# Optimization experiments

Measured on AMD Instinct MI355X. Metric: run time of the kernel, lower is better.

Reference implementation:

```python
import jax, jax.numpy as jnp
import numpy as np

N, E, IN, H0, H1 = 50000, 1600000, 64, 64, 128


def _gcn(h, W, b, row, col):
    # PyG GCNConv, add_self_loops=False, unit edge weights:
    # out[col] += d^{-1/2}[row] * d^{-1/2}[col] * (h @ W)[row]; bias added after aggregation
    n = h.shape[0]
    deg = jnp.zeros((n,), h.dtype).at[col].add(jnp.ones((row.shape[0],), h.dtype))
    dinv = jnp.where(deg > 0, jax.lax.rsqrt(jnp.maximum(deg, 1e-12)), 0.0)
    norm = (dinv[row] * dinv[col])[:, None]  # [E,1]
    m = h @ W  # transform before propagate (small GEMM)
    out = jnp.zeros((n, W.shape[1]), h.dtype).at[col].add(norm * m[row])
    return out + b


def _bn(h, g, b):
    # BatchNorm1d training-mode math (biased variance), eps=1e-5
    mu = h.mean(0)
    var = ((h - mu) ** 2).mean(0)
    return g * (h - mu) * jax.lax.rsqrt(var + 1e-5) + b


def _san(h):
    return jnp.nan_to_num(h, nan=0.0, posinf=100.0, neginf=-100.0)


def _slice(x, ei, W0, b0, W1, b1, res1, g0, be0, g1, be1):
    row, col = ei[0], ei[1]
    # layer 0: conv -> bn -> relu -> (dropout=eval identity) -> residual (Identity, 64==64) -> nan_to_num
    h1 = _san(jax.nn.relu(_bn(_gcn(x, W0, b0, row, col), g0, be0)) + x)
    # layer 1 (last): conv -> bn -> residual (Linear proj 64->128, no bias) -> nan_to_num
    h2 = _san(_bn(_gcn(h1, W1, b1, row, col), g1, be1) + h1 @ res1)
    return h2


def setup_inputs() -> dict:
    k = jax.random.split(jax.random.key(0), 16)
    f = lambda kk, sh, s: jax.random.normal(kk, sh, jnp.float32) * s
    return {
        "x": f(k[0], (N, IN), 1.0),
        "edge_index0": jax.random.randint(k[1], (2, E), 0, N),
        "edge_index1": jax.random.randint(k[2], (2, E), 0, N),
        "w0_s0": f(k[3], (IN, H0), 0.1), "b0_s0": jnp.zeros((H0,), jnp.float32),
        "w1_s0": f(k[4], (H0, H1), 0.1), "b1_s0": jnp.zeros((H1,), jnp.float32),
        "res1_s0": f(k[5], (H0, H1), 0.1),
        "w0_s1": f(k[6], (IN, H0), 0.1), "b0_s1": jnp.zeros((H0,), jnp.float32),
        "w1_s1": f(k[7], (H0, H1), 0.1), "b1_s1": jnp.zeros((H1,), jnp.float32),
        "res1_s1": f(k[8], (H0, H1), 0.1),
        "bn_g0": jnp.ones((H0,), jnp.float32), "bn_b0": jnp.zeros((H0,), jnp.float32),
        "bn_g1": jnp.ones((H1,), jnp.float32), "bn_b1": jnp.zeros((H1,), jnp.float32),
        "fc1_w": f(k[9], (2 * H1, H1), 0.1), "fc1_b": jnp.zeros((H1,), jnp.float32),
        "fc2_w": f(k[10], (H1, 2), 0.1), "fc2_b": jnp.zeros((2,), jnp.float32),
    }


def reference(x, edge_index0, edge_index1,
              w0_s0, b0_s0, w1_s0, b1_s0, res1_s0,
              w0_s1, b0_s1, w1_s1, b1_s1, res1_s1,
              bn_g0, bn_b0, bn_g1, bn_b1,
              fc1_w, fc1_b, fc2_w, fc2_b):
    out0 = _slice(x, edge_index0, w0_s0, b0_s0, w1_s0, b1_s0, res1_s0, bn_g0, bn_b0, bn_g1, bn_b1)
    out1 = _slice(x, edge_index1, w0_s1, b0_s1, w1_s1, b1_s1, res1_s1, bn_g0, bn_b0, bn_g1, bn_b1)
    combined = jnp.concatenate([out0, out1], axis=1)  # [N, 2*H1]
    h = jax.nn.relu(combined @ fc1_w + fc1_b)  # dropout is eval-mode identity
    logits = h @ fc2_w + fc2_b
    return logits, jax.nn.softmax(logits, axis=1)
```

## Files before the change

### kernel.cpp

```cpp
#include <hip/hip_runtime.h>
#include <hip/hip_bf16.h>
#include <math.h>


typedef short v8s __attribute__((ext_vector_type(8)));
typedef float f32x4 __attribute__((ext_vector_type(4)));

#define BSTRIDE 10240

__device__ __forceinline__ float sanf(float v) {
    if (v != v) return 0.f;
    if (isinf(v)) return v > 0.f ? 100.f : -100.f;
    return v;
}

__device__ __forceinline__ unsigned short bf16of(float v) {
    __hip_bfloat16 h = __float2bfloat16(v);
    return *(unsigned short*)&h;
}
__device__ __forceinline__ unsigned pack2(float lo, float hi) {
    return (unsigned)bf16of(lo) | ((unsigned)bf16of(hi) << 16);
}
__device__ __forceinline__ float uflo(unsigned u) { return __uint_as_float(u << 16); }
__device__ __forceinline__ float ufhi(unsigned u) { return __uint_as_float(u & 0xFFFF0000u); }
__device__ __forceinline__ float fofbf16(unsigned short u) {
    return __uint_as_float(((unsigned)u) << 16);
}

__device__ __forceinline__ void packone(const float* __restrict__ src, unsigned* __restrict__ dst,
                                        int L, int Khalf, int F) {
    int c = L / Khalf, kp = L - c * Khalf;
    dst[L] = pack2(src[(2 * kp) * F + c], src[(2 * kp + 1) * F + c]);
}

__global__ __launch_bounds__(256) void prep_kernel(const float* __restrict__ w0_0,
                                                   const float* __restrict__ w0_1,
                                                   const float* __restrict__ w1_0,
                                                   const float* __restrict__ w1_1,
                                                   const float* __restrict__ r_0,
                                                   const float* __restrict__ r_1,
                                                   const float* __restrict__ fc1,
                                                   unsigned* __restrict__ wpk,
                                                   int* __restrict__ bcnt,
                                                   float* __restrict__ sums) {
    int gid = blockIdx.x * 256 + threadIdx.x;
    if (gid < 512) bcnt[gid] = 0;
    if (gid < 8192) sums[gid] = 0.f;
    if (gid < 2048)       packone(w0_0, wpk + 0,     gid - 0,     32, 64);
    else if (gid < 4096)  packone(w0_1, wpk + 2048,  gid - 2048,  32, 64);
    else if (gid < 8192)  packone(w1_0, wpk + 4096,  gid - 4096,  32, 128);
    else if (gid < 12288) packone(w1_1, wpk + 8192,  gid - 8192,  32, 128);
    else if (gid < 16384) packone(r_0,  wpk + 12288, gid - 12288, 32, 128);
    else if (gid < 20480) packone(r_1,  wpk + 16384, gid - 16384, 32, 128);
    else if (gid < 36864) packone(fc1,  wpk + 20480, gid - 20480, 128, 128);
}


__global__ __launch_bounds__(512) void kC_bin(const int* __restrict__ ei0,
                                              const int* __restrict__ ei1,
                                              int* __restrict__ bcnt,
                                              unsigned* __restrict__ binned,
                                              int E, int n) {
    __shared__ int cnt[512];
    __shared__ int base[512];
    int t = threadIdx.x;
    cnt[t] = 0;
    int E2 = 2 * E;
    int e0 = blockIdx.x * 8192;
    unsigned pk[16];
    int bk[16];
    __syncthreads();
#pragma unroll
    for (int j = 0; j < 16; ++j) {
        int ge = e0 + t + j * 512;
        bk[j] = -1;
        if (ge < E2) {
            int slice = ge >= E;
            const int* ei = slice ? ei1 : ei0;
            int e = ge - slice * E;
            int col = ei[E + e], row = ei[e];
            int gcol = slice * n + col;
            bk[j] = gcol >> 8;
            pk[j] = (unsigned)row | (((unsigned)gcol & 255u) << 16);
            atomicAdd(&cnt[bk[j]], 1);
        }
    }
    __syncthreads();
    {
        int c = cnt[t];
        base[t] = c ? atomicAdd(&bcnt[t], c) : 0;
    }
    __syncthreads();
    cnt[t] = 0;
    __syncthreads();
#pragma unroll
    for (int j = 0; j < 16; ++j) {
        if (bk[j] >= 0) {
            int loc = atomicAdd(&cnt[bk[j]], 1);
            int off = base[bk[j]] + loc;
            if (off < BSTRIDE) binned[(size_t)bk[j] * BSTRIDE + off] = pk[j];
        }
    }
}

__global__ __launch_bounds__(512) void kD_build(const unsigned* __restrict__ binned,
                                                const int* __restrict__ bcnt,
                                                int* __restrict__ rowptr,
                                                float* __restrict__ dinv,
                                                unsigned short* __restrict__ csr,
                                                int n2, int NB) {
    __shared__ int pref[512];
    __shared__ int cnt[256];
    __shared__ int scn[256];
    __shared__ int cur[256];
    int b = blockIdx.x, t = threadIdx.x;
    pref[t] = (t < NB) ? bcnt[t] : 0;
    __syncthreads();
    for (int off = 1; off < 512; off <<= 1) {
        int u = (t >= off) ? pref[t - off] : 0;
        __syncthreads();
        pref[t] += u;
        __syncthreads();
    }
    int s = (b > 0) ? pref[b - 1] : 0;
    int e = pref[b];
    int m = e - s;
    const unsigned* seg = binned + (size_t)b * BSTRIDE;
    if (t < 256) cnt[t] = 0;
    __syncthreads();
    for (int i = t; i < m; i += 512) atomicAdd(&cnt[(seg[i] >> 16) & 255], 1);
    __syncthreads();
    int v = (t < 256) ? cnt[t] : 0;
    if (t < 256) scn[t] = v;
    __syncthreads();
    for (int off = 1; off < 256; off <<= 1) {
        int u = (t < 256 && t >= off) ? scn[t - off] : 0;
        __syncthreads();
        if (t < 256) scn[t] += u;
        __syncthreads();
    }
    if (t < 256) {
        int excl = scn[t] - v;
        int gcol = b * 256 + t;
        if (gcol < n2) {
            rowptr[gcol] = s + excl;
            dinv[gcol] = v > 0 ? rsqrtf((float)v) : 0.f;
        }
        cur[t] = excl;
    }
    __syncthreads();
    for (int i = t; i < m; i += 512) {
        unsigned p = seg[i];
        int cl = (p >> 16) & 255;
        int pos = s + atomicAdd(&cur[cl], 1);
        csr[pos] = (unsigned short)(p & 0xFFFFu);
    }
    if (b == 0 && t == 0) rowptr[n2] = pref[NB - 1];
}


__global__ __launch_bounds__(256) void prescale_bf(const float* __restrict__ x,
                                                   const float* __restrict__ dinv,
                                                   unsigned short* __restrict__ xsb,
                                                   int n64, int n) {
    int i8 = (blockIdx.x * 256 + threadIdx.x) * 8;
    if (i8 >= n64) return;
    int row = i8 >> 6;
    float4 v0 = *(const float4*)&x[i8];
    float4 v1 = *(const float4*)&x[i8 + 4];
    float d0 = dinv[row], d1 = dinv[n + row];
    uint4 o0, o1;
    o0.x = pack2(v0.x * d0, v0.y * d0); o0.y = pack2(v0.z * d0, v0.w * d0);
    o0.z = pack2(v1.x * d0, v1.y * d0); o0.w = pack2(v1.z * d0, v1.w * d0);
    o1.x = pack2(v0.x * d1, v0.y * d1); o1.y = pack2(v0.z * d1, v0.w * d1);
    o1.z = pack2(v1.x * d1, v1.y * d1); o1.w = pack2(v1.z * d1, v1.w * d1);
    *(uint4*)&xsb[i8] = o0;
    *(uint4*)&xsb[n64 + i8] = o1;
}

#define LOAD8(U, IDX)                                                       \
    do {                                                                    \
        _Pragma("unroll") for (int j = 0; j < 8; ++j) {                     \
            int r = __shfl((IDX), j, 8);                                    \
            (U)[j] = *(const uint4*)&mb[(size_t)r * 64 + l * 8];            \
        }                                                                   \
    } while (0)
#define ZPAD8(U, BB)                                                        \
    do {                                                                    \
        _Pragma("unroll") for (int j = 0; j < 8; ++j)                       \
            if ((BB) + j >= e) { (U)[j].x = 0; (U)[j].y = 0;                \
                                 (U)[j].z = 0; (U)[j].w = 0; }              \
    } while (0)
#define ACC8(U)                                                             \
    do {                                                                    \
        _Pragma("unroll") for (int j = 0; j < 8; ++j) {                     \
            a0 += uflo((U)[j].x); a1 += ufhi((U)[j].x);                     \
            a2 += uflo((U)[j].y); a3 += ufhi((U)[j].y);                     \
            a4 += uflo((U)[j].z); a5 += ufhi((U)[j].z);                     \
            a6 += uflo((U)[j].w); a7 += ufhi((U)[j].w);                     \
        }                                                                   \
    } while (0)

__device__ __forceinline__ void gather_node(const int* __restrict__ rowptr,
                                            const unsigned short* __restrict__ csr,
                                            const unsigned short* __restrict__ mb,
                                            const float* __restrict__ dinv,
                                            int node, int l,
                                            unsigned short* __restrict__ dstrow) {
    int s = rowptr[node], e = rowptr[node + 1];
    float a0 = 0.f, a1 = 0.f, a2 = 0.f, a3 = 0.f, a4 = 0.f, a5 = 0.f, a6 = 0.f, a7 = 0.f;
    uint4 uA[8], uB[8];
    int b = s;
    if (b + 8 <= e) {
        int ia = csr[b + l];
        LOAD8(uA, ia);
        int bB = b + 8;
        int ib = (bB + l < e) ? (int)csr[bB + l] : 0;
        while (true) {
            bool hasB = (bB < e);
            if (hasB) {
                LOAD8(uB, ib);
                if (bB + 8 > e) ZPAD8(uB, bB);
            }
            int bA2 = bB + 8;
            if (bA2 < e) ia = (bA2 + l < e) ? (int)csr[bA2 + l] : 0;
            ACC8(uA);
            if (!hasB) break;
            bool hasA2 = (bA2 < e);
            if (hasA2) {
                LOAD8(uA, ia);
                if (bA2 + 8 > e) ZPAD8(uA, bA2);
            }
            int bB2 = bA2 + 8;
            if (bB2 < e) ib = (bB2 + l < e) ? (int)csr[bB2 + l] : 0;
            ACC8(uB);
            if (!hasA2) break;
            bB = bB2;
        }
    } else if (b < e) {
        int ia = (b + l < e) ? (int)csr[b + l] : 0;
        LOAD8(uA, ia);
        ZPAD8(uA, b);
        ACC8(uA);
    }
    float d = dinv[node];
    uint4 o;
    o.x = pack2(a0 * d, a1 * d);
    o.y = pack2(a2 * d, a3 * d);
    o.z = pack2(a4 * d, a5 * d);
    o.w = pack2(a6 * d, a7 * d);
    *(uint4*)&dstrow[l * 8] = o;
}

template <int F>
__global__ __launch_bounds__(256) void gather_gemmb(const int* __restrict__ rowptr,
                                                    const unsigned short* __restrict__ csr,
                                                    const unsigned short* __restrict__ xsb,
                                                    const float* __restrict__ dinv,
                                                    const unsigned* __restrict__ WT0,
                                                    const unsigned* __restrict__ WT1,
                                                    unsigned short* __restrict__ Cb,
                                                    float* __restrict__ sums_base,
                                                    int roff, int n, int BPS) {
    constexpr int NC = F / 16;
    __shared__ unsigned short at[64 * 72];
    __shared__ unsigned short stb[64 * F];
    __shared__ float ls[2 * F];
    int blk = blockIdx.x;
    int xcd = blk & 7;
    int slice = (xcd >= 4) ? 1 : 0;
    int sb = (blk >> 3) * 4 + (xcd & 3);
    if (sb >= BPS) return;
    const unsigned* WT = slice ? WT1 : WT0;
    int row0 = slice * n + sb * 64;
    int rows = min(64, n - sb * 64);
    int grp = threadIdx.x >> 3, l = threadIdx.x & 7;
    const unsigned short* mb = xsb + (size_t)slice * n * 64;
#pragma unroll
    for (int half = 0; half < 2; ++half) {
        int lr = grp + half * 32;
        if (lr < rows) {
            gather_node(rowptr, csr, mb, dinv, row0 + lr, l, &at[lr * 72]);
        } else {
            uint4 z; z.x = 0; z.y = 0; z.z = 0; z.w = 0;
            *(uint4*)&at[lr * 72 + l * 8] = z;
        }
    }
    for (int i = threadIdx.x; i < 2 * F; i += 256) ls[i] = 0.f;
    __syncthreads();
    int w = threadIdx.x >> 6, lane = threadIdx.x & 63, q = lane >> 4, ln = lane & 15;
    int arow = (16 * w + ln) * 72;
    v8s af0 = *(const v8s*)&at[arow + q * 8];
    v8s af1 = *(const v8s*)&at[arow + 32 + q * 8];
    f32x4 acc[NC];
#pragma unroll
    for (int ct = 0; ct < NC; ++ct) acc[ct] = {0.f, 0.f, 0.f, 0.f};
#pragma unroll
    for (int ct = 0; ct < NC; ++ct) {
        v8s b0 = *(const v8s*)&WT[(ct * 16 + ln) * 32 + q * 4];
        v8s b1 = *(const v8s*)&WT[(ct * 16 + ln) * 32 + 16 + q * 4];
        acc[ct] = __builtin_amdgcn_mfma_f32_16x16x32_bf16(af0, b0, acc[ct], 0, 0, 0);
        acc[ct] = __builtin_amdgcn_mfma_f32_16x16x32_bf16(af1, b1, acc[ct], 0, 0, 0);
    }
#pragma unroll
    for (int ct = 0; ct < NC; ++ct) {
        float s1 = 0.f, s2 = 0.f;
        int cc = ct * 16 + ln;
#pragma unroll
        for (int i = 0; i < 4; ++i) {
            int r = 16 * w + q * 4 + i;
            stb[r * F + (cc ^ ((r & 7) << 3))] = bf16of(acc[ct][i]);
            if (r < rows) {
                float v = acc[ct][i];
                s1 += v;
                s2 += v * v;
            }
        }
        s1 += __shfl_xor(s1, 16); s1 += __shfl_xor(s1, 32);
        s2 += __shfl_xor(s2, 16); s2 += __shfl_xor(s2, 32);
        if (q == 0) {
            atomicAdd(&ls[cc], s1);
            atomicAdd(&ls[F + cc], s2);
        }
    }
    __syncthreads();
    {
        constexpr int CPT = F / 4;
        int rr = threadIdx.x >> 2, sg = threadIdx.x & 3;
        if (rr < rows) {
            int swz = (rr & 7) << 3;
            int cb = sg * CPT;
            uint4* dst = (uint4*)(Cb + (size_t)(row0 + rr) * F + cb);
#pragma unroll
            for (int jj = 0; jj < CPT / 8; ++jj)
                dst[jj] = *(const uint4*)&stb[rr * F + ((cb + jj * 8) ^ swz)];
        }
    }
    if (threadIdx.x < F) {
        float* dst = sums_base + (blockIdx.x & 7) * 1024 + roff + slice * 2 * F;
        unsafeAtomicAdd(&dst[threadIdx.x], ls[threadIdx.x]);
        unsafeAtomicAdd(&dst[F + threadIdx.x], ls[F + threadIdx.x]);
    }
}

__global__ __launch_bounds__(256) void mfma_apply1(const unsigned short* __restrict__ h1b,
                                                   const unsigned short* __restrict__ Tb,
                                                   const unsigned* __restrict__ RT0,
                                                   const unsigned* __restrict__ RT1,
                                                   const float* __restrict__ sums_base,
                                                   const float* __restrict__ g,
                                                   const float* __restrict__ be,
                                                   unsigned short* __restrict__ comb, int n) {
    __shared__ float st[64 * 128];
    __shared__ float scl[256];
    int BPS = (n + 63) >> 6;
    int slice = blockIdx.x >= BPS;
    int sb = blockIdx.x - slice * BPS;
    const unsigned* WT = slice ? RT1 : RT0;
    int row0 = slice * n + sb * 64;
    int rows = min(64, n - sb * 64);
    int t = threadIdx.x;
    if (t < 128) {
        float s1 = 0.f, s2 = 0.f;
#pragma unroll
        for (int r = 0; r < 8; ++r) {
            const float* src = sums_base + r * 1024 + slice * 256;
            s1 += src[t];
            s2 += src[128 + t];
        }
        float inv_n = 1.0f / (float)n;
        float mu = s1 * inv_n;
        float var = fmaxf(s2 * inv_n - mu * mu, 0.f);
        float scale = g[t] * rsqrtf(var + 1e-5f);
        scl[t] = scale;
        scl[128 + t] = be[t] - mu * scale;
    }
    int w = t >> 6, lane = t & 63, q = lane >> 4, ln = lane & 15;
    const unsigned* A32 = (const unsigned*)h1b;
    size_t arow = (size_t)(row0 + 16 * w + ln) * 32;
    v8s af0 = *(const v8s*)&A32[arow + q * 4];
    v8s af1 = *(const v8s*)&A32[arow + 16 + q * 4];
    f32x4 acc[8];
#pragma unroll
    for (int ct = 0; ct < 8; ++ct) acc[ct] = {0.f, 0.f, 0.f, 0.f};
#pragma unroll
    for (int ct = 0; ct < 8; ++ct) {
        v8s b0 = *(const v8s*)&WT[(ct * 16 + ln) * 32 + q * 4];
        v8s b1 = *(const v8s*)&WT[(ct * 16 + ln) * 32 + 16 + q * 4];
        acc[ct] = __builtin_amdgcn_mfma_f32_16x16x32_bf16(af0, b0, acc[ct], 0, 0, 0);
        acc[ct] = __builtin_amdgcn_mfma_f32_16x16x32_bf16(af1, b1, acc[ct], 0, 0, 0);
    }
#pragma unroll
    for (int ct = 0; ct < 8; ++ct) {
        int cc = ct * 16 + ln;
#pragma unroll
        for (int i = 0; i < 4; ++i) {
            int r = 16 * w + q * 4 + i;
            st[r * 128 + (cc ^ ((r & 7) << 2))] = acc[ct][i];
        }
    }
    __syncthreads();
    int rr = t >> 2, sg = t & 3;
    if (rr >= rows) return;
    int swz = (rr & 7) << 2;
    int rg = row0 + rr;
    const uint4* tbp = (const uint4*)(Tb + (size_t)rg * 128 + sg * 32);
    const float* scb = scl + sg * 32;
    uint4* outp = (uint4*)(comb + (size_t)(rg - slice * n) * 256 + slice * 128 + sg * 32);
#pragma unroll
    for (int jj = 0; jj < 4; ++jj) {
        uint4 tv = tbp[jj];
        int base = sg * 32 + jj * 8;
        float4 a0 = *(const float4*)&st[rr * 128 + (base ^ swz)];
        float4 a1 = *(const float4*)&st[rr * 128 + ((base + 4) ^ swz)];
        float4 s0 = *(const float4*)&scb[jj * 8];
        float4 s1 = *(const float4*)&scb[jj * 8 + 4];
        float4 h0 = *(const float4*)&scb[128 + jj * 8];
        float4 h1v = *(const float4*)&scb[128 + jj * 8 + 4];
        float o0 = sanf(fmaf(uflo(tv.x), s0.x, h0.x) + a0.x);
        float o1 = sanf(fmaf(ufhi(tv.x), s0.y, h0.y) + a0.y);
        float o2 = sanf(fmaf(uflo(tv.y), s0.z, h0.z) + a0.z);
        float o3 = sanf(fmaf(ufhi(tv.y), s0.w, h0.w) + a0.w);
        float o4 = sanf(fmaf(uflo(tv.z), s1.x, h1v.x) + a1.x);
        float o5 = sanf(fmaf(ufhi(tv.z), s1.y, h1v.y) + a1.y);
        float o6 = sanf(fmaf(uflo(tv.w), s1.z, h1v.z) + a1.z);
        float o7 = sanf(fmaf(ufhi(tv.w), s1.w, h1v.w) + a1.w);
        uint4 ov;
        ov.x = pack2(o0, o1);
        ov.y = pack2(o2, o3);
        ov.z = pack2(o4, o5);
        ov.w = pack2(o6, o7);
        outp[jj] = ov;
    }
}

__global__ __launch_bounds__(256) void mfma_head_fc2(const unsigned short* __restrict__ comb,
                                                     const unsigned* __restrict__ FT,
                                                     const float* __restrict__ bias,
                                                     const float* __restrict__ w2,
                                                     const float* __restrict__ b2,
                                                     float* __restrict__ out, int n) {
    int row0 = blockIdx.x * 64;
    int rows = min(64, n - row0);
    int w = threadIdx.x >> 6, lane = threadIdx.x & 63, q = lane >> 4, ln = lane & 15;
    const unsigned* A32 = (const unsigned*)comb;
    size_t arow = (size_t)(row0 + 16 * w + ln) * 128;
    f32x4 acc[8];
#pragma unroll
    for (int ct = 0; ct < 8; ++ct) acc[ct] = {0.f, 0.f, 0.f, 0.f};
#pragma unroll
    for (int kt = 0; kt < 4; ++kt) {
        v8s af0 = *(const v8s*)&A32[arow + kt * 32 + q * 4];
        v8s af1 = *(const v8s*)&A32[arow + kt * 32 + 16 + q * 4];
#pragma unroll
        for (int ct = 0; ct < 8; ++ct) {
            v8s b0 = *(const v8s*)&FT[(ct * 16 + ln) * 128 + kt * 32 + q * 4];
            v8s b1 = *(const v8s*)&FT[(ct * 16 + ln) * 128 + kt * 32 + 16 + q * 4];
            acc[ct] = __builtin_amdgcn_mfma_f32_16x16x32_bf16(af0, b0, acc[ct], 0, 0, 0);
            acc[ct] = __builtin_amdgcn_mfma_f32_16x16x32_bf16(af1, b1, acc[ct], 0, 0, 0);
        }
    }
    float p0[4] = {0.f, 0.f, 0.f, 0.f}, p1[4] = {0.f, 0.f, 0.f, 0.f};
#pragma unroll
    for (int ct = 0; ct < 8; ++ct) {
        int c = ct * 16 + ln;
        float bi = bias[c];
        float w20 = w2[c * 2], w21 = w2[c * 2 + 1];
#pragma unroll
        for (int i = 0; i < 4; ++i) {
            float h = fmaxf(acc[ct][i] + bi, 0.f);
            p0[i] = fmaf(h, w20, p0[i]);
            p1[i] = fmaf(h, w21, p1[i]);
        }
    }
#pragma unroll
    for (int i = 0; i < 4; ++i) {
#pragma unroll
        for (int msk = 1; msk < 16; msk <<= 1) {
            p0[i] += __shfl_xor(p0[i], msk);
            p1[i] += __shfl_xor(p1[i], msk);
        }
    }
    if (ln == 0) {
        float bb0 = b2[0], bb1 = b2[1];
#pragma unroll
        for (int i = 0; i < 4; ++i) {
            int r = 16 * w + q * 4 + i;
            if (r >= rows) continue;
            int R = row0 + r;
            float l0 = p0[i] + bb0, l1 = p1[i] + bb1;
            float mx = fmaxf(l0, l1);
            float e0 = expf(l0 - mx), e1 = expf(l1 - mx);
            float inv = 1.0f / (e0 + e1);
            out[(size_t)R * 2] = l0;
            out[(size_t)R * 2 + 1] = l1;
            out[(size_t)2 * n + R * 2] = e0 * inv;
            out[(size_t)2 * n + R * 2 + 1] = e1 * inv;
        }
    }
}

__global__ __launch_bounds__(256) void apply0_kernel(const unsigned short* __restrict__ t0b,
                                                     const float* __restrict__ x,
                                                     const float* __restrict__ sums_base,
                                                     const float* __restrict__ g,
                                                     const float* __restrict__ be,
                                                     const float* __restrict__ dinv,
                                                     unsigned short* __restrict__ h1b,
                                                     unsigned short* __restrict__ h1sb,
                                                     int n64, int total, int n) {
    __shared__ float sc[256];
    int t = threadIdx.x;
    if (t < 128) {
        int slice = t >> 6, f = t & 63;
        float s1 = 0.f, s2 = 0.f;
#pragma unroll
        for (int r = 0; r < 8; ++r) {
            const float* src = sums_base + r * 1024 + 512 + slice * 128;
            s1 += src[f];
            s2 += src[64 + f];
        }
        float inv_n = 1.0f / (float)n;
        float mu = s1 * inv_n;
        float var = fmaxf(s2 * inv_n - mu * mu, 0.f);
        float scale = g[f] * rsqrtf(var + 1e-5f);
        sc[slice * 128 + f] = scale;
        sc[slice * 128 + 64 + f] = be[f] - mu * scale;
    }
    __syncthreads();
    int i8 = (blockIdx.x * 256 + t) * 8;
    if (i8 >= total) return;
    int slice = i8 >= n64;
    int f0 = i8 & 63;
    const float* scp = sc + slice * 128;
    uint4 tv = *(const uint4*)&t0b[i8];
    const float* xp = x + (i8 - slice * n64);
    float4 x0 = *(const float4*)xp;
    float4 x1 = *(const float4*)(xp + 4);
    float4 s0 = *(const float4*)&scp[f0];
    float4 s1 = *(const float4*)&scp[f0 + 4];
    float4 g0 = *(const float4*)&scp[64 + f0];
    float4 g1 = *(const float4*)&scp[64 + f0 + 4];
    float d = dinv[i8 >> 6];
    float tvv[8] = {uflo(tv.x), ufhi(tv.x), uflo(tv.y), ufhi(tv.y),
                    uflo(tv.z), ufhi(tv.z), uflo(tv.w), ufhi(tv.w)};
    float sa[8] = {s0.x, s0.y, s0.z, s0.w, s1.x, s1.y, s1.z, s1.w};
    float sh[8] = {g0.x, g0.y, g0.z, g0.w, g1.x, g1.y, g1.z, g1.w};
    float xv[8] = {x0.x, x0.y, x0.z, x0.w, x1.x, x1.y, x1.z, x1.w};
    unsigned po[4], ps[4];
#pragma unroll
    for (int j = 0; j < 4; ++j) {
        float a = sanf(fmaxf(fmaf(tvv[2 * j], sa[2 * j], sh[2 * j]), 0.f) + xv[2 * j]);
        float b = sanf(fmaxf(fmaf(tvv[2 * j + 1], sa[2 * j + 1], sh[2 * j + 1]), 0.f) + xv[2 * j + 1]);
        po[j] = pack2(a, b);
        ps[j] = pack2(a * d, b * d);
    }
    *(uint4*)&h1b[i8] = *(uint4*)po;
    *(uint4*)&h1sb[i8] = *(uint4*)ps;
}

static inline int cdiv(int a, int b) { return (a + b - 1) / b; }

extern "C" void kernel_launch(void* const* d_in, const int* in_sizes, int n_in,
                              void* d_out, int out_size, void* d_ws, size_t ws_size,
                              hipStream_t stream) {
    const float* x       = (const float*)d_in[0];
    const int*   ei0     = (const int*)d_in[1];
    const int*   ei1     = (const int*)d_in[2];
    const float* w0_s0   = (const float*)d_in[3];
    const float* w1_s0   = (const float*)d_in[5];
    const float* res1_s0 = (const float*)d_in[7];
    const float* w0_s1   = (const float*)d_in[8];
    const float* w1_s1   = (const float*)d_in[10];
    const float* res1_s1 = (const float*)d_in[12];
    const float* bn_g0   = (const float*)d_in[13];
    const float* bn_b0   = (const float*)d_in[14];
    const float* bn_g1   = (const float*)d_in[15];
    const float* bn_b1   = (const float*)d_in[16];
    const float* fc1_w   = (const float*)d_in[17];
    const float* fc1_b   = (const float*)d_in[18];
    const float* fc2_w   = (const float*)d_in[19];
    const float* fc2_b   = (const float*)d_in[20];
    float* out = (float*)d_out;

    int n = in_sizes[0] / 64;
    int E = in_sizes[1] / 2;
    int n2 = 2 * n, E2 = 2 * E;
    int n64 = n * 64;
    int NB = cdiv(n2, 256);
    int BPS = cdiv(n, 64);
    int GG = 8 * cdiv(BPS, 4);

    float* X1 = (float*)d_ws;
    float* S  = X1 + (size_t)n2 * 64;
    unsigned short* Gb   = (unsigned short*)(S + (size_t)n2 * 64);
    unsigned short* h1b  = Gb + (size_t)n2 * 64;
    unsigned short* comb = h1b + (size_t)n2 * 64;
    unsigned short* xsb  = comb + (size_t)n * 256;
    float* dinv = (float*)(xsb + (size_t)n * 128);
    float* sums = dinv + n2;
    float* scsh = sums + 8192;
    unsigned* wpk = (unsigned*)(scsh + 512);
    unsigned short* csr = (unsigned short*)(wpk + 36864);
    int* rowptr = (int*)(csr + (size_t)E2);
    int* bcnt   = rowptr + (n2 + 1);
    unsigned short* t0b = (unsigned short*)X1;
    unsigned short* Tb  = (unsigned short*)X1;
    unsigned* binned = (unsigned*)comb;
    unsigned short* h1sb = (unsigned short*)S;
    unsigned* w0T0 = wpk + 0,    *w0T1 = wpk + 2048;
    unsigned* w1T0 = wpk + 4096, *w1T1 = wpk + 8192;
    unsigned* rT0  = wpk + 12288,*rT1  = wpk + 16384;
    unsigned* fT   = wpk + 20480;

    prep_kernel<<<144, 256, 0, stream>>>(w0_s0, w0_s1, w1_s0, w1_s1,
                                         res1_s0, res1_s1, fc1_w, wpk, bcnt, sums);
    kC_bin<<<cdiv(E2, 8192), 512, 0, stream>>>(ei0, ei1, bcnt, binned, E, n);
    kD_build<<<NB, 512, 0, stream>>>(binned, bcnt, rowptr, dinv, csr, n2, NB);

    prescale_bf<<<cdiv(n64, 2048), 256, 0, stream>>>(x, dinv, xsb, n64, n);
    gather_gemmb<64><<<GG, 256, 0, stream>>>(rowptr, csr, xsb, dinv, w0T0, w0T1,
                                             t0b, sums, 512, n, BPS);
    apply0_kernel<<<cdiv(2 * n64, 2048), 256, 0, stream>>>(t0b, x, sums, bn_g0, bn_b0,
                                                           dinv, h1b, h1sb, n64, 2 * n64, n);

    gather_gemmb<128><<<GG, 256, 0, stream>>>(rowptr, csr, h1sb, dinv, w1T0, w1T1,
                                              Tb, sums, 0, n, BPS);
    mfma_apply1<<<2 * BPS, 256, 0, stream>>>(h1b, Tb, rT0, rT1, sums, bn_g1, bn_b1, comb, n);

    mfma_head_fc2<<<BPS, 256, 0, stream>>>(comb, fT, fc1_b, fc2_w, fc2_b, out, n);
}
```

Baseline: 371.1 us.

## Split fused gather+GEMM into separate gather kernel and MFMA GEMM kernel

Replaces the fused gather_gemmb kernel, which gathered neighbour rows into LDS and then ran MFMA, with two kernels: a standalone gather kernel that writes the aggregated bf16 rows to a global buffer, and an MFMA GEMM that reads A fragments straight from global memory. The gather now runs at 32 nodes per block with no LDS, which may raise occupancy and decouple the latency-bound gather from the GEMM. In exchange it adds an extra global round trip for the aggregated features and two more kernel launches.

```diff
diff --git a/kernel.cpp b/kernel.cpp
--- a/kernel.cpp
+++ b/kernel.cpp
@@ -201,12 +201,21 @@
         }                                                                   \
     } while (0)
 
-__device__ __forceinline__ void gather_node(const int* __restrict__ rowptr,
-                                            const unsigned short* __restrict__ csr,
-                                            const unsigned short* __restrict__ mb,
-                                            const float* __restrict__ dinv,
-                                            int node, int l,
-                                            unsigned short* __restrict__ dstrow) {
+__global__ __launch_bounds__(256) void gatherbf_kernel(const int* __restrict__ rowptr,
+                                                       const unsigned short* __restrict__ csr,
+                                                       const unsigned short* __restrict__ xsb,
+                                                       const float* __restrict__ dinv,
+                                                       unsigned short* __restrict__ outb,
+                                                       int n) {
+    int blk = blockIdx.x;
+    int xcd = blk & 7;
+    int slice = (xcd >= 4) ? 1 : 0;
+    int rank = (blk >> 3) * 4 + (xcd & 3);
+    int nodeLocal = rank * 32 + (threadIdx.x >> 3);
+    if (nodeLocal >= n) return;
+    int node = slice * n + nodeLocal;
+    int l = threadIdx.x & 7;
+    const unsigned short* mb = xsb + (size_t)slice * n * 64;
     int s = rowptr[node], e = rowptr[node + 1];
     float a0 = 0.f, a1 = 0.f, a2 = 0.f, a3 = 0.f, a4 = 0.f, a5 = 0.f, a6 = 0.f, a7 = 0.f;
     uint4 uA[8], uB[8];
@@ -249,49 +258,32 @@
     o.y = pack2(a2 * d, a3 * d);
     o.z = pack2(a4 * d, a5 * d);
     o.w = pack2(a6 * d, a7 * d);
-    *(uint4*)&dstrow[l * 8] = o;
-}
+    *(uint4*)&outb[(size_t)node * 64 + l * 8] = o;
+}
+
 
 template <int F>
-__global__ __launch_bounds__(256) void gather_gemmb(const int* __restrict__ rowptr,
-                                                    const unsigned short* __restrict__ csr,
-                                                    const unsigned short* __restrict__ xsb,
-                                                    const float* __restrict__ dinv,
-                                                    const unsigned* __restrict__ WT0,
-                                                    const unsigned* __restrict__ WT1,
-                                                    unsigned short* __restrict__ Cb,
-                                                    float* __restrict__ sums_base,
-                                                    int roff, int n, int BPS) {
+__global__ __launch_bounds__(256) void mfma_gemmb(const unsigned short* __restrict__ Ab,
+                                                  const unsigned* __restrict__ WT0,
+                                                  const unsigned* __restrict__ WT1,
+                                                  unsigned short* __restrict__ Cb,
+                                                  float* __restrict__ sums_base,
+                                                  int roff, int n) {
     constexpr int NC = F / 16;
-    __shared__ unsigned short at[64 * 72];
+    __shared__ float ls[2 * F];
     __shared__ unsigned short stb[64 * F];
-    __shared__ float ls[2 * F];
-    int blk = blockIdx.x;
-    int xcd = blk & 7;
-    int slice = (xcd >= 4) ? 1 : 0;
-    int sb = (blk >> 3) * 4 + (xcd & 3);
-    if (sb >= BPS) return;
+    int BPS = (n + 63) >> 6;
+    int slice = blockIdx.x >= BPS;
+    int sb = blockIdx.x - slice * BPS;
     const unsigned* WT = slice ? WT1 : WT0;
     int row0 = slice * n + sb * 64;
     int rows = min(64, n - sb * 64);
-    int grp = threadIdx.x >> 3, l = threadIdx.x & 7;
-    const unsigned short* mb = xsb + (size_t)slice * n * 64;
-#pragma unroll
-    for (int half = 0; half < 2; ++half) {
-        int lr = grp + half * 32;
-        if (lr < rows) {
-            gather_node(rowptr, csr, mb, dinv, row0 + lr, l, &at[lr * 72]);
-        } else {
-            uint4 z; z.x = 0; z.y = 0; z.z = 0; z.w = 0;
-            *(uint4*)&at[lr * 72 + l * 8] = z;
-        }
-    }
     for (int i = threadIdx.x; i < 2 * F; i += 256) ls[i] = 0.f;
-    __syncthreads();
     int w = threadIdx.x >> 6, lane = threadIdx.x & 63, q = lane >> 4, ln = lane & 15;
-    int arow = (16 * w + ln) * 72;
-    v8s af0 = *(const v8s*)&at[arow + q * 8];
-    v8s af1 = *(const v8s*)&at[arow + 32 + q * 8];
+    const unsigned* A32 = (const unsigned*)Ab;
+    size_t arow = (size_t)(row0 + 16 * w + ln) * 32;
+    v8s af0 = *(const v8s*)&A32[arow + q * 4];
+    v8s af1 = *(const v8s*)&A32[arow + 16 + q * 4];
     f32x4 acc[NC];
 #pragma unroll
     for (int ct = 0; ct < NC; ++ct) acc[ct] = {0.f, 0.f, 0.f, 0.f};
@@ -302,6 +294,7 @@
         acc[ct] = __builtin_amdgcn_mfma_f32_16x16x32_bf16(af0, b0, acc[ct], 0, 0, 0);
         acc[ct] = __builtin_amdgcn_mfma_f32_16x16x32_bf16(af1, b1, acc[ct], 0, 0, 0);
     }
+    __syncthreads();
 #pragma unroll
     for (int ct = 0; ct < NC; ++ct) {
         float s1 = 0.f, s2 = 0.f;
@@ -589,7 +582,7 @@
     int n64 = n * 64;
     int NB = cdiv(n2, 256);
     int BPS = cdiv(n, 64);
-    int GG = 8 * cdiv(BPS, 4);
+    int GB = 8 * cdiv(cdiv(n, 32), 4);
 
     float* X1 = (float*)d_ws;
     float* S  = X1 + (size_t)n2 * 64;
@@ -619,13 +612,13 @@
     kD_build<<<NB, 512, 0, stream>>>(binned, bcnt, rowptr, dinv, csr, n2, NB);
 
     prescale_bf<<<cdiv(n64, 2048), 256, 0, stream>>>(x, dinv, xsb, n64, n);
-    gather_gemmb<64><<<GG, 256, 0, stream>>>(rowptr, csr, xsb, dinv, w0T0, w0T1,
-                                             t0b, sums, 512, n, BPS);
+    gatherbf_kernel<<<GB, 256, 0, stream>>>(rowptr, csr, xsb, dinv, Gb, n);
+    mfma_gemmb<64><<<2 * BPS, 256, 0, stream>>>(Gb, w0T0, w0T1, t0b, sums, 512, n);
     apply0_kernel<<<cdiv(2 * n64, 2048), 256, 0, stream>>>(t0b, x, sums, bn_g0, bn_b0,
                                                            dinv, h1b, h1sb, n64, 2 * n64, n);
 
-    gather_gemmb<128><<<GG, 256, 0, stream>>>(rowptr, csr, h1sb, dinv, w1T0, w1T1,
-                                              Tb, sums, 0, n, BPS);
+    gatherbf_kernel<<<GB, 256, 0, stream>>>(rowptr, csr, h1sb, dinv, Gb, n);
+    mfma_gemmb<128><<<2 * BPS, 256, 0, stream>>>(Gb, w1T0, w1T1, Tb, sums, 0, n);
     mfma_apply1<<<2 * BPS, 256, 0, stream>>>(h1b, Tb, rT0, rT1, sums, bn_g1, bn_b1, comb, n);
 
     mfma_head_fc2<<<BPS, 256, 0, stream>>>(comb, fT, fc1_b, fc2_w, fc2_b, out, n);
```

Measured after the change: 353.5 us. -4.8%, faster.
